# Optimization experiments

Measured on AMD Instinct MI355X. Metric: run time of the kernel, lower is better.

Reference implementation:

```python
import jax, jax.numpy as jnp
import numpy as np
from jax import lax

NMODES, STEP, DTAPS, NTAPS = 2, 5, 1001, 101
HID = 100
L_FIBER = 2000000.0
DZ = L_FIBER / STEP
GAMMA = 0.0016567
D_PARAM = 16.5
FC = 299792458.0 / 1.55e-6
FS_NOM = 160e9
B, SEQ = 4, 500000


def _get_beta2(D, Fc):
    c_kms = 299792458.0 / 1e3  # speed of light [km/s]
    lamb = c_kms / Fc          # wavelength [km]
    return -(D * lamb ** 2) / (2.0 * np.pi * c_kms)


def _dispersion_kernel(Fs):
    # Fs: [B] sampling rate in Hz -> time-domain dispersion kernel [B, DTAPS] complex64
    beta2 = _get_beta2(D_PARAM, FC) / 1000.0  # [s^2/m]
    beta1 = 0.0  # Fi == Fc so the walk-off term vanishes
    dz = -DZ     # module calls dispersion_kernel(-self.dz, ...)
    f = np.fft.fftfreq(DTAPS).astype(np.float32)
    omega = 2.0 * np.pi * Fs[:, None] * f  # [B, DTAPS] rad/s
    phase = (beta2 / 2.0) * omega ** 2 * dz + beta1 * omega * dz
    kf = jnp.exp(-1j * phase)  # freq-domain response, complex64
    return jnp.fft.fftshift(jnp.fft.ifft(kf, axis=-1), axes=-1).astype(jnp.complex64)


def _nonlinear_kernel(task_info, W1, b1, W2, b2):
    # hypernetwork-generated nonlinear kernel [B, NMODES, NMODES, NTAPS]
    scale = 1.0 / 200.0
    b = task_info.shape[0]
    Fs = task_info[:, 2] / FS_NOM
    Ts = (1.0 / Fs)[:, None, None]  # [B,1,1] (broadcasts over taps like expand)
    pos = jnp.abs(jnp.arange(-(NTAPS // 2), NTAPS // 2 + 1)).astype(jnp.float32)
    pos = pos[None, :, None] * scale  # [1,NTAPS,1]
    inp = pos * Ts ** 2               # [B,NTAPS,1]
    h = jax.nn.relu(inp @ W1 + b1)    # [B,NTAPS,HID]
    mlp_out = h @ W2 + b2             # [B,NTAPS,NMODES^2]
    k1 = Ts ** 2 * mlp_out * jnp.exp(-pos * Ts ** 2)
    return jnp.transpose(k1, (0, 2, 1)).reshape(b, NMODES, NMODES, NTAPS)


def _corr(x, h):
    # x:[B,M,L] real, h:[B,taps] -> valid cross-correlation [B,M,L-taps+1] (torch conv1d semantics)
    def one(xb, hb):
        return lax.conv_general_dilated(xb[:, None, :], hb[None, None, :], (1,), 'VALID')[:, 0]
    return jax.vmap(one)(x, h)


def _nconv(p, K):
    # p:[B,Min,L], K:[B,Mout,Min,taps] -> [B,Mout,L-taps+1]
    def one(pb, Kb):
        return lax.conv_general_dilated(pb[None], Kb, (1,), 'VALID')[0]
    return jax.vmap(one)(p, K)


def _forward(x_real, x_imag, task_info, W1, b1, W2, b2):
    P = 0.001 * 10.0 ** (task_info[:, 0] / 10.0) / NMODES  # launch power per mode [W]
    Dk = _dispersion_kernel(task_info[:, 2])
    hr, hi = jnp.real(Dk), jnp.imag(Dk)
    Nk = _nonlinear_kernel(task_info, W1, b1, W2, b2)
    xr = jnp.transpose(x_real, (0, 2, 1))  # [B,M,L]
    xi = jnp.transpose(x_imag, (0, 2, 1))
    trim = (NTAPS - 1) // 2
    coef = (GAMMA * DZ) * P[:, None, None]
    for _ in range(STEP):
        # complex dispersion conv: (xr+i xi) * (hr+i hi)
        ar = _corr(xr, hr) - _corr(xi, hi)
        ai = _corr(xr, hi) + _corr(xi, hr)
        # nonlinear phase from |x|^2 filtered by hypernet kernel
        phi = _nconv(ar ** 2 + ai ** 2, Nk)  # [B,M,L-ntaps+1]
        theta = phi * coef
        c, s = jnp.cos(theta), jnp.sin(theta)
        art = ar[:, :, trim:ar.shape[2] - trim]
        ait = ai[:, :, trim:ai.shape[2] - trim]
        # x * exp(i*theta)
        xr = art * c - ait * s
        xi = art * s + ait * c
    out = jnp.stack([xr, xi], axis=-1)      # [B,M,Lout,2]
    return jnp.transpose(out, (0, 2, 1, 3))  # [B,Lout,M,2] (real/imag stacked)


def setup_inputs() -> dict:
    key = jax.random.key(0)
    k = jax.random.split(key, 6)
    x_real = jax.random.normal(k[0], (B, SEQ, NMODES), jnp.float32)
    x_imag = jax.random.normal(k[1], (B, SEQ, NMODES), jnp.float32)
    Pdbm = jax.random.uniform(k[2], (B,), jnp.float32, -2.0, 2.0)
    task_info = jnp.stack([Pdbm,
                           jnp.full((B,), FC, jnp.float32),
                           jnp.full((B,), FS_NOM, jnp.float32),
                           jnp.ones((B,), jnp.float32)], axis=1)
    W1 = jax.random.normal(k[3], (1, HID), jnp.float32) * 0.5
    b1 = jnp.zeros((HID,), jnp.float32)
    W2 = jax.random.normal(k[4], (HID, NMODES * NMODES), jnp.float32) * 0.02
    b2 = jnp.zeros((NMODES * NMODES,), jnp.float32)
    return {"x_real": x_real, "x_imag": x_imag, "task_info": task_info,
            "W1": W1, "b1": b1, "W2": W2, "b2": b2}


def reference(x_real, x_imag, task_info, W1, b1, W2, b2):
    return _forward(x_real, x_imag, task_info, W1, b1, W2, b2)
```

## Files before the change

### kernel.cpp

```cpp
#include <hip/hip_runtime.h>

#define NM      2
#define STEPS_C 5
#define DTAPS_C 1001
#define NTAPS_C 101
#define HID_C   100
#define B_C     4
#define SEQ_C   500000
#define SSTR    SEQ_C
#define NKP     104
#define FS_NOM_D 160000000000.0
#define PI_D 3.14159265358979323846

#define SWZ(L) ((L) + ((((unsigned)(L)) >> 5) << 2))

#define LD4V(A0,A1,A2,A3, SRC) { float4 q_ = *(const float4*)&(SRC); \
    A0=q_.x; A1=q_.y; A2=q_.z; A3=q_.w; }

__device__ __forceinline__ void cmulf(float& o_r, float& o_i,
                                      float a_r, float a_i, float b_r, float b_i)
{ o_r = a_r * b_r - a_i * b_i; o_i = a_r * b_i + a_i * b_r; }

__global__ void build_disp(const float* __restrict__ task,
                           float* __restrict__ HR, float* __restrict__ HI)
{
    __shared__ double skr[DTAPS_C], ski[DTAPS_C];
    const int b = blockIdx.y;
    const double Fs = (double)task[b * 4 + 2];
    const double c_kms = 299792458.0 / 1000.0;
    const double Fc    = 299792458.0 / 1.55e-6;
    const double lamb  = c_kms / Fc;
    const double beta2 = -(16.5 * lamb * lamb) / (2.0 * PI_D * c_kms) / 1000.0;
    const double dz    = -400000.0;

    for (int k = threadIdx.x; k < DTAPS_C; k += blockDim.x) {
        double fk = ((k <= DTAPS_C / 2) ? (double)k : (double)(k - DTAPS_C)) / (double)DTAPS_C;
        double om = 2.0 * PI_D * Fs * fk;
        double ph = 0.5 * beta2 * om * om * dz;
        ph = fmod(ph, 2.0 * PI_D);
        double s, c; sincos(ph, &s, &c);
        skr[k] = c;  ski[k] = -s;
    }
    __syncthreads();

    const int ln = threadIdx.x >> 3;
    const int kp = threadIdx.x & 7;
    const int n  = blockIdx.x * 32 + ln;
    double dr = 0.0, di = 0.0;
    {
        const int nn = (n < DTAPS_C) ? n : 0;
        const int r0 = (nn * kp) % DTAPS_C;
        const int rs = (nn * 8) % DTAPS_C;
        double a0 = 2.0 * PI_D * (double)r0 / (double)DTAPS_C;
        double as = 2.0 * PI_D * (double)rs / (double)DTAPS_C;
        double s0, c0, ss, cs;
        sincos(a0, &s0, &c0);
        sincos(as, &ss, &cs);
        for (int k = kp; k < DTAPS_C; k += 8) {
            dr += skr[k] * c0 - ski[k] * s0;
            di += skr[k] * s0 + ski[k] * c0;
            const double nc = c0 * cs - s0 * ss;
            s0 = c0 * ss + s0 * cs;
            c0 = nc;
        }
    }
    #pragma unroll
    for (int m = 1; m <= 4; m <<= 1) {
        dr += __shfl_xor(dr, m, 64);
        di += __shfl_xor(di, m, 64);
    }
    if (kp == 0 && n < DTAPS_C) {
        int m = n + DTAPS_C / 2; if (m >= DTAPS_C) m -= DTAPS_C;
        HR[b * DTAPS_C + m] = (float)(dr / (double)DTAPS_C);
        HI[b * DTAPS_C + m] = (float)(di / (double)DTAPS_C);
    }
}

__global__ void build_G(const float* __restrict__ HR, const float* __restrict__ HI,
                        float* __restrict__ Gb)
{
    __shared__ float shr[DTAPS_C], shi[DTAPS_C];
    const int b = blockIdx.y;
    for (int k = threadIdx.x; k < DTAPS_C; k += blockDim.x) {
        shr[k] = HR[b * DTAPS_C + k];
        shi[k] = HI[b * DTAPS_C + k];
    }
    __syncthreads();

    const int ln = threadIdx.x >> 3;
    const int kp = threadIdx.x & 7;
    const int f  = blockIdx.x * 32 + ln;
    double ar = 0.0, ai = 0.0;
    {
        const int r0 = (f * kp) & 4095;
        const int rs = (f * 8) & 4095;
        double a0 = (2.0 * PI_D / 4096.0) * (double)r0;
        double as = (2.0 * PI_D / 4096.0) * (double)rs;
        double s0, c0, ss, cs;
        sincos(a0, &s0, &c0);
        sincos(as, &ss, &cs);
        for (int k = kp; k < DTAPS_C; k += 8) {
            const double hre = (double)shr[k], him = (double)shi[k];
            ar += hre * c0 - him * s0;
            ai += hre * s0 + him * c0;
            const double nc = c0 * cs - s0 * ss;
            s0 = c0 * ss + s0 * cs;
            c0 = nc;
        }
    }
    #pragma unroll
    for (int m = 1; m <= 4; m <<= 1) {
        ar += __shfl_xor(ar, m, 64);
        ai += __shfl_xor(ai, m, 64);
    }
    if (kp == 0) {
        const int p = ((f & 15) << 8) + (((f >> 4) & 15) << 4) + (f >> 8);
        Gb[(size_t)(b * 4096 + p) * 2 + 0] = (float)(ar * (1.0 / 4096.0));
        Gb[(size_t)(b * 4096 + p) * 2 + 1] = (float)(ai * (1.0 / 4096.0));
    }
}

__global__ void build_nk(const float* __restrict__ task,
                         const float* __restrict__ W1, const float* __restrict__ b1,
                         const float* __restrict__ W2, const float* __restrict__ b2,
                         float* __restrict__ NKg, float* __restrict__ COEF)
{
    const int tid = threadIdx.x;
    for (int i = tid; i < B_C * 4 * NKP; i += blockDim.x) NKg[i] = 0.f;
    if (tid < B_C) {
        float pdbm = task[tid * 4 + 0];
        float P = 0.001f * powf(10.f, pdbm * 0.1f) / (float)NM;
        COEF[tid] = (float)(0.0016567 * 400000.0) * P;
    }
    __syncthreads();
    if (tid < B_C * NTAPS_C) {
        const int b = tid / NTAPS_C, tap = tid % NTAPS_C;
        float Fsn = task[b * 4 + 2] * (float)(1.0 / FS_NOM_D);
        float Ts = 1.f / Fsn, Ts2 = Ts * Ts;
        float pos = fabsf((float)(tap - NTAPS_C / 2)) * (1.f / 200.f);
        float inp = pos * Ts2;
        float o0 = b2[0], o1 = b2[1], o2 = b2[2], o3 = b2[3];
        for (int j = 0; j < HID_C; ++j) {
            float h = fmaxf(fmaf(inp, W1[j], b1[j]), 0.f);
            o0 = fmaf(h, W2[j * 4 + 0], o0);
            o1 = fmaf(h, W2[j * 4 + 1], o1);
            o2 = fmaf(h, W2[j * 4 + 2], o2);
            o3 = fmaf(h, W2[j * 4 + 3], o3);
        }
        float sc = Ts2 * expf(-pos * Ts2);
        NKg[(b * 4 + 0) * NKP + tap] = o0 * sc;
        NKg[(b * 4 + 1) * NKP + tap] = o1 * sc;
        NKg[(b * 4 + 2) * NKP + tap] = o2 * sc;
        NKg[(b * 4 + 3) * NKP + tap] = o3 * sc;
    }
}

__global__ void transpose_in(const float* __restrict__ xr_in, const float* __restrict__ xi_in,
                             float* __restrict__ XR, float* __restrict__ XI)
{
    int idx = blockIdx.x * blockDim.x + threadIdx.x;
    if (idx >= B_C * SEQ_C) return;
    int b = idx / SEQ_C, t = idx - b * SEQ_C;
    float2 vr = ((const float2*)xr_in)[idx];
    float2 vi = ((const float2*)xi_in)[idx];
    XR[(size_t)(b * 2 + 0) * SSTR + t] = vr.x;
    XR[(size_t)(b * 2 + 1) * SSTR + t] = vr.y;
    XI[(size_t)(b * 2 + 0) * SSTR + t] = vi.x;
    XI[(size_t)(b * 2 + 1) * SSTR + t] = vi.y;
}

template<int SGN>
__device__ __forceinline__ void dft4(float& ar, float& ai, float& br, float& bi,
                                     float& cr, float& ci, float& dr, float& di)
{
    float t0r = ar + cr, t0i = ai + ci;
    float t1r = ar - cr, t1i = ai - ci;
    float t2r = br + dr, t2i = bi + di;
    float t3r = br - dr, t3i = bi - di;
    ar = t0r + t2r; ai = t0i + t2i;
    cr = t0r - t2r; ci = t0i - t2i;
    if (SGN < 0) {
        br = t1r + t3i; bi = t1i - t3r;
        dr = t1r - t3i; di = t1i + t3r;
    } else {
        br = t1r - t3i; bi = t1i + t3r;
        dr = t1r + t3i; di = t1i - t3r;
    }
}

template<int SGN>
__device__ __forceinline__ void tw16(float& r, float& i, float c, float s)
{
    float nr, ni;
    if (SGN < 0) { nr = r * c + i * s; ni = i * c - r * s; }
    else         { nr = r * c - i * s; ni = i * c + r * s; }
    r = nr; i = ni;
}

template<int SGN>
__device__ __forceinline__ void dft16(float (&xr)[16], float (&xi)[16])
{
    #pragma unroll
    for (int n1 = 0; n1 < 4; ++n1)
        dft4<SGN>(xr[n1], xi[n1], xr[n1+4], xi[n1+4],
                  xr[n1+8], xi[n1+8], xr[n1+12], xi[n1+12]);
    const float C1 = 0.923879532511286756f, S1 = 0.382683432365089772f;
    const float C2 = 0.707106781186547524f;
    tw16<SGN>(xr[5],  xi[5],  C1,  S1);
    tw16<SGN>(xr[9],  xi[9],  C2,  C2);
    tw16<SGN>(xr[13], xi[13], S1,  C1);
    tw16<SGN>(xr[6],  xi[6],  C2,  C2);
    tw16<SGN>(xr[10], xi[10], 0.f, 1.f);
    tw16<SGN>(xr[14], xi[14], -C2, C2);
    tw16<SGN>(xr[7],  xi[7],  S1,  C1);
    tw16<SGN>(xr[11], xi[11], -C2, C2);
    tw16<SGN>(xr[15], xi[15], -C1, -S1);
    #pragma unroll
    for (int k4 = 0; k4 < 4; ++k4)
        dft4<SGN>(xr[4*k4+0], xi[4*k4+0], xr[4*k4+1], xi[4*k4+1],
                  xr[4*k4+2], xi[4*k4+2], xr[4*k4+3], xi[4*k4+3]);
}

#define TWLADDER_INIT(c_, s_)                                              \
    float w1r_ = (c_), w1i_ = (s_), w2r_, w2i_, w3r_, w3i_, w4r_, w4i_;    \
    cmulf(w2r_, w2i_, w1r_, w1i_, w1r_, w1i_);                             \
    cmulf(w3r_, w3i_, w2r_, w2i_, w1r_, w1i_);                             \
    cmulf(w4r_, w4i_, w2r_, w2i_, w2r_, w2i_);                             \
    float bgr_ = 1.f, bgi_ = 0.f;

#define TWLADDER_GET(k_, twr_, twi_)                                       \
    {                                                                      \
        const int j_ = (k_) & 3;                                           \
        if      (j_ == 0) { twr_ = bgr_; twi_ = bgi_; }                    \
        else if (j_ == 1) cmulf(twr_, twi_, bgr_, bgi_, w1r_, w1i_);       \
        else if (j_ == 2) cmulf(twr_, twi_, bgr_, bgi_, w2r_, w2i_);       \
        else              cmulf(twr_, twi_, bgr_, bgi_, w3r_, w3i_);       \
    }

#define TWLADDER_STEP(k_)                                                  \
    if (((k_) & 3) == 3 && (k_) < 15) {                                    \
        float nr_, ni_;                                                    \
        cmulf(nr_, ni_, bgr_, bgi_, w4r_, w4i_);                           \
        bgr_ = nr_; bgi_ = ni_;                                            \
    }

#define FFTN  4096
#define FSTEP 3096
#define PH(i) ((i) + ((((unsigned)(i)) >> 5) << 1))
#define LDSN  4352

__global__ __launch_bounds__(256, 2) void disp_fft(
    const float* __restrict__ XR, const float* __restrict__ XI,
    const float* __restrict__ Gb,
    float* __restrict__ AR, float* __restrict__ AI, int La)
{
    __shared__ __align__(16) float sre[LDSN];
    __shared__ __align__(16) float sim[LDSN];
    const int t = threadIdx.x;
    const int seq = blockIdx.y;
    const int b = seq >> 1;
    const int tile0 = blockIdx.x * FSTEP;
    const int Lin = La + (DTAPS_C - 1);
    const int rem_in = Lin - tile0;
    const float* xr = XR + (size_t)seq * SSTR + tile0;
    const float* xi = XI + (size_t)seq * SSTR + tile0;

    #pragma unroll
    for (int q = 0; q < 4; ++q) {
        const int i0 = q * 1024 + t * 4;
        float4 vr4 = make_float4(0.f, 0.f, 0.f, 0.f);
        float4 vi4 = make_float4(0.f, 0.f, 0.f, 0.f);
        if (i0 + 3 < rem_in) {
            vr4 = *(const float4*)(xr + i0);
            vi4 = *(const float4*)(xi + i0);
        } else {
            if (i0 + 0 < rem_in) { vr4.x = xr[i0+0]; vi4.x = xi[i0+0]; }
            if (i0 + 1 < rem_in) { vr4.y = xr[i0+1]; vi4.y = xi[i0+1]; }
            if (i0 + 2 < rem_in) { vr4.z = xr[i0+2]; vi4.z = xi[i0+2]; }
        }
        const int p = PH(i0);
        sre[p+0] = vr4.x; sre[p+1] = vr4.y; sre[p+2] = vr4.z; sre[p+3] = vr4.w;
        sim[p+0] = vi4.x; sim[p+1] = vi4.y; sim[p+2] = vi4.z; sim[p+3] = vi4.w;
    }
    __syncthreads();

    float vr[16], vi[16];

    {
        const int base = PH(t);
        #pragma unroll
        for (int m = 0; m < 16; ++m) { vr[m] = sre[base + 272*m]; vi[m] = sim[base + 272*m]; }
        dft16<-1>(vr, vi);
        float s, c; sincosf((float)(-2.0 * PI_D / 4096.0) * (float)t, &s, &c);
        TWLADDER_INIT(c, s)
        #pragma unroll
        for (int k = 0; k < 16; ++k) {
            const int sl = 4*(k&3) + (k>>2);
            float twr, twi;
            TWLADDER_GET(k, twr, twi)
            sre[base + 272*k] = vr[sl]*twr - vi[sl]*twi;
            sim[base + 272*k] = vr[sl]*twi + vi[sl]*twr;
            TWLADDER_STEP(k)
        }
    }
    __syncthreads();

    {
        const int j = t & 15, blk = t >> 4;
        const int base = 272*blk + j;
        #pragma unroll
        for (int m = 0; m < 16; ++m) {
            const int o = base + 16*m + 2*(m>>1);
            vr[m] = sre[o]; vi[m] = sim[o];
        }
        dft16<-1>(vr, vi);
        float s, c; sincosf((float)(-2.0 * PI_D / 256.0) * (float)j, &s, &c);
        TWLADDER_INIT(c, s)
        #pragma unroll
        for (int k = 0; k < 16; ++k) {
            const int sl = 4*(k&3) + (k>>2);
            const int o = base + 16*k + 2*(k>>1);
            float twr, twi;
            TWLADDER_GET(k, twr, twi)
            sre[o] = vr[sl]*twr - vi[sl]*twi;
            sim[o] = vr[sl]*twi + vi[sl]*twr;
            TWLADDER_STEP(k)
        }
    }
    __syncthreads();

    {
        const int base = 16*t + 2*(t>>1);
        #pragma unroll
        for (int m = 0; m < 16; ++m) { vr[m] = sre[base + m]; vi[m] = sim[base + m]; }
        dft16<-1>(vr, vi);
        const float2* gp = ((const float2*)Gb) + ((size_t)b << 12) + (t << 4);
        float wr2[16], wi2[16];
        #pragma unroll
        for (int k = 0; k < 16; ++k) {
            const int sl = 4*(k&3) + (k>>2);
            const float2 g = gp[k];
            wr2[k] = vr[sl]*g.x - vi[sl]*g.y;
            wi2[k] = vr[sl]*g.y + vi[sl]*g.x;
        }
        dft16<1>(wr2, wi2);
        #pragma unroll
        for (int m = 0; m < 16; ++m) {
            const int sl = 4*(m&3) + (m>>2);
            sre[base + m] = wr2[sl]; sim[base + m] = wi2[sl];
        }
    }
    __syncthreads();

    {
        const int j = t & 15, blk = t >> 4;
        const int base = 272*blk + j;
        float s, c; sincosf((float)(2.0 * PI_D / 256.0) * (float)j, &s, &c);
        TWLADDER_INIT(c, s)
        #pragma unroll
        for (int k = 0; k < 16; ++k) {
            const int o = base + 16*k + 2*(k>>1);
            const float a = sre[o], d = sim[o];
            float twr, twi;
            TWLADDER_GET(k, twr, twi)
            vr[k] = a*twr - d*twi; vi[k] = a*twi + d*twr;
            TWLADDER_STEP(k)
        }
        dft16<1>(vr, vi);
        #pragma unroll
        for (int m = 0; m < 16; ++m) {
            const int sl = 4*(m&3) + (m>>2);
            const int o = base + 16*m + 2*(m>>1);
            sre[o] = vr[sl]; sim[o] = vi[sl];
        }
    }
    __syncthreads();

    {
        const int base = PH(t);
        float s, c; sincosf((float)(2.0 * PI_D / 4096.0) * (float)t, &s, &c);
        TWLADDER_INIT(c, s)
        #pragma unroll
        for (int k = 0; k < 16; ++k) {
            const float a = sre[base + 272*k], d = sim[base + 272*k];
            float twr, twi;
            TWLADDER_GET(k, twr, twi)
            vr[k] = a*twr - d*twi; vi[k] = a*twi + d*twr;
            TWLADDER_STEP(k)
        }
        dft16<1>(vr, vi);
        #pragma unroll
        for (int m = 0; m < 16; ++m) {
            const int sl = 4*(m&3) + (m>>2);
            sre[base + 272*m] = vr[sl]; sim[base + 272*m] = vi[sl];
        }
    }
    __syncthreads();

    const int nout = min(FSTEP, La - tile0);
    float* arp = AR + (size_t)seq * SSTR + tile0;
    float* aip = AI + (size_t)seq * SSTR + tile0;
    #pragma unroll
    for (int q = 0; q < 4; ++q) {
        const int i0 = q * 1024 + t * 4;
        if (i0 >= nout) continue;
        const int p = PH(i0);
        if (i0 + 3 < nout) {
            *(float4*)(arp + i0) = make_float4(sre[p], sre[p+1], sre[p+2], sre[p+3]);
            *(float4*)(aip + i0) = make_float4(sim[p], sim[p+1], sim[p+2], sim[p+3]);
        } else {
            for (int k = 0; k < 4; ++k) if (i0 + k < nout) {
                arp[i0+k] = sre[p+k]; aip[i0+k] = sim[p+k];
            }
        }
    }
}

#define K2_BLOCK 256
#define K2_TILE  2048
#define K2_LDSL  2176
#define K2_LDSP  2448

#define N_CH8(W_, V_, N_, P0, P1, KK)                                      \
  {                                                                        \
    LD4V(N_[0],N_[1],N_[2],N_[3], sp[P0]);                                 \
    LD4V(N_[4],N_[5],N_[6],N_[7], sp[P1]);                                 \
    _Pragma("unroll")                                                      \
    for (int d = 0; d < 8; ++d) {                                          \
      const float av = nkA[(KK) + d], bv = nkB[(KK) + d];                  \
      _Pragma("unroll")                                                    \
      for (int j = 0; j < 8; ++j) {                                        \
        const float xv = (j + d < 8) ? W_[j + d] : V_[j + d - 8];          \
        th0[j] = fmaf(av, xv, th0[j]);                                     \
        th1[j] = fmaf(bv, xv, th1[j]);                                     \
      }                                                                    \
    }                                                                      \
  }

__global__ __launch_bounds__(K2_BLOCK, 4) void nl_rotate(
    const float* __restrict__ AR, const float* __restrict__ AI,
    const float* __restrict__ NKg, const float* __restrict__ COEF,
    float* __restrict__ XR, float* __restrict__ XI,
    float* __restrict__ OUT, int Lb, int finalstep)
{
    __shared__ __align__(16) float sp0[K2_LDSP];
    __shared__ __align__(16) float sp1[K2_LDSP];
    const int b = blockIdx.y;
    const int tile0 = blockIdx.x * K2_TILE;
    const int nout  = min(K2_TILE, Lb - tile0);
    const int cnt   = nout + NTAPS_C - 1;
    const float* ar0 = AR + (size_t)(2 * b + 0) * SSTR + tile0;
    const float* ai0 = AI + (size_t)(2 * b + 0) * SSTR + tile0;
    const float* ar1 = AR + (size_t)(2 * b + 1) * SSTR + tile0;
    const float* ai1 = AI + (size_t)(2 * b + 1) * SSTR + tile0;

    for (int i0 = threadIdx.x * 4; i0 < K2_LDSL; i0 += K2_BLOCK * 4) {
        float4 p0v = make_float4(0.f, 0.f, 0.f, 0.f);
        float4 p1v = make_float4(0.f, 0.f, 0.f, 0.f);
        if (i0 + 3 < cnt) {
            float4 a4 = *(const float4*)(ar0 + i0);
            float4 c4 = *(const float4*)(ai0 + i0);
            float4 d4 = *(const float4*)(ar1 + i0);
            float4 e4 = *(const float4*)(ai1 + i0);
            p0v.x = fmaf(a4.x, a4.x, c4.x * c4.x);
            p0v.y = fmaf(a4.y, a4.y, c4.y * c4.y);
            p0v.z = fmaf(a4.z, a4.z, c4.z * c4.z);
            p0v.w = fmaf(a4.w, a4.w, c4.w * c4.w);
            p1v.x = fmaf(d4.x, d4.x, e4.x * e4.x);
            p1v.y = fmaf(d4.y, d4.y, e4.y * e4.y);
            p1v.z = fmaf(d4.z, d4.z, e4.z * e4.z);
            p1v.w = fmaf(d4.w, d4.w, e4.w * e4.w);
        } else {
            float p0a[4] = {0.f, 0.f, 0.f, 0.f};
            float p1a[4] = {0.f, 0.f, 0.f, 0.f};
            #pragma unroll
            for (int u = 0; u < 4; ++u) {
                const int i = i0 + u;
                if (i < cnt) {
                    float a = ar0[i], c = ai0[i];
                    float d = ar1[i], e = ai1[i];
                    p0a[u] = fmaf(a, a, c * c);
                    p1a[u] = fmaf(d, d, e * e);
                }
            }
            p0v = make_float4(p0a[0], p0a[1], p0a[2], p0a[3]);
            p1v = make_float4(p1a[0], p1a[1], p1a[2], p1a[3]);
        }
        const int p = SWZ(i0);
        *(float4*)&sp0[p] = p0v;
        *(float4*)&sp1[p] = p1v;
    }

    const int t0 = threadIdx.x * 8;
    float ra0[8], rb0[8], ra1[8], rb1[8];
    {
        const float* art0 = ar0 + t0 + NTAPS_C / 2;
        const float* ait0 = ai0 + t0 + NTAPS_C / 2;
        const float* art1 = ar1 + t0 + NTAPS_C / 2;
        const float* ait1 = ai1 + t0 + NTAPS_C / 2;
        #pragma unroll
        for (int j = 0; j < 8; ++j) {
            ra0[j] = art0[j]; rb0[j] = ait0[j];
            ra1[j] = art1[j]; rb1[j] = ait1[j];
        }
    }
    __syncthreads();

    if (t0 >= nout) return;

    float th0[8], th1[8];
    #pragma unroll
    for (int j = 0; j < 8; ++j) { th0[j] = 0.f; th1[j] = 0.f; }
    const float* nkb = NKg + b * 4 * NKP;

    const int a0 = SWZ(t0 + 16), a1 = SWZ(t0 + 20), a2 = SWZ(t0 + 24), a3 = SWZ(t0 + 28);
    const int a4 = SWZ(t0 + 32), a5 = SWZ(t0 + 36), a6 = SWZ(t0 + 40), a7 = SWZ(t0 + 44);

    for (int im = 0; im < 2; ++im) {
        const float* sp  = im ? sp1 : sp0;
        const float* nkA = nkb + (0 * 2 + im) * NKP;
        const float* nkB = nkb + (1 * 2 + im) * NKP;
        float U[8], V[8], N[8];
        LD4V(U[0],U[1],U[2],U[3], sp[SWZ(t0)]);
        LD4V(U[4],U[5],U[6],U[7], sp[SWZ(t0 + 4)]);
        LD4V(V[0],V[1],V[2],V[3], sp[SWZ(t0 + 8)]);
        LD4V(V[4],V[5],V[6],V[7], sp[SWZ(t0 + 12)]);
        N_CH8(U, V, N, a0,       a1,        0);
        N_CH8(V, N, U, a2,       a3,        8);
        N_CH8(N, U, V, a4,       a5,       16);
        N_CH8(U, V, N, a6,       a7,       24);
        N_CH8(V, N, U, a0 + 36,  a1 + 36,  32);
        N_CH8(N, U, V, a2 + 36,  a3 + 36,  40);
        N_CH8(U, V, N, a4 + 36,  a5 + 36,  48);
        N_CH8(V, N, U, a6 + 36,  a7 + 36,  56);
        N_CH8(N, U, V, a0 + 72,  a1 + 72,  64);
        N_CH8(U, V, N, a2 + 72,  a3 + 72,  72);
        N_CH8(V, N, U, a4 + 72,  a5 + 72,  80);
        N_CH8(N, U, V, a6 + 72,  a7 + 72,  88);
        N_CH8(U, V, N, a0 + 108, a1 + 108, 96);
    }

    const float coef = COEF[b];
    const int tg = tile0 + t0;

    float or0[8], oi0[8], or1[8], oi1[8];
    #pragma unroll
    for (int j = 0; j < 8; ++j) {
        float s0, c0, s1, c1;
        sincosf(th0[j] * coef, &s0, &c0);
        sincosf(th1[j] * coef, &s1, &c1);
        float a0v = ra0[j], b0v = rb0[j];
        float a1v = ra1[j], b1v = rb1[j];
        or0[j] = fmaf(a0v, c0, -b0v * s0);
        oi0[j] = fmaf(a0v, s0,  b0v * c0);
        or1[j] = fmaf(a1v, c1, -b1v * s1);
        oi1[j] = fmaf(a1v, s1,  b1v * c1);
    }

    const int rem = nout - t0;
    if (finalstep) {
        float4* op = (float4*)(OUT + (size_t)(b * Lb + tg) * 4);
        if (rem >= 8) {
            #pragma unroll
            for (int j = 0; j < 8; ++j) op[j] = make_float4(or0[j], oi0[j], or1[j], oi1[j]);
        } else {
            for (int j = 0; j < rem; ++j) op[j] = make_float4(or0[j], oi0[j], or1[j], oi1[j]);
        }
    } else {
        float* xr0 = XR + (size_t)(2 * b + 0) * SSTR + tg;
        float* xi0 = XI + (size_t)(2 * b + 0) * SSTR + tg;
        float* xr1 = XR + (size_t)(2 * b + 1) * SSTR + tg;
        float* xi1 = XI + (size_t)(2 * b + 1) * SSTR + tg;
        if (rem >= 8) {
            ((float4*)xr0)[0] = make_float4(or0[0], or0[1], or0[2], or0[3]);
            ((float4*)xr0)[1] = make_float4(or0[4], or0[5], or0[6], or0[7]);
            ((float4*)xi0)[0] = make_float4(oi0[0], oi0[1], oi0[2], oi0[3]);
            ((float4*)xi0)[1] = make_float4(oi0[4], oi0[5], oi0[6], oi0[7]);
            ((float4*)xr1)[0] = make_float4(or1[0], or1[1], or1[2], or1[3]);
            ((float4*)xr1)[1] = make_float4(or1[4], or1[5], or1[6], or1[7]);
            ((float4*)xi1)[0] = make_float4(oi1[0], oi1[1], oi1[2], oi1[3]);
            ((float4*)xi1)[1] = make_float4(oi1[4], oi1[5], oi1[6], oi1[7]);
        } else {
            for (int j = 0; j < rem; ++j) {
                xr0[j] = or0[j]; xi0[j] = oi0[j];
                xr1[j] = or1[j]; xi1[j] = oi1[j];
            }
        }
    }
}

extern "C" void kernel_launch(void* const* d_in, const int* in_sizes, int n_in,
                              void* d_out, int out_size, void* d_ws, size_t ws_size,
                              hipStream_t stream)
{
    const float* x_real = (const float*)d_in[0];
    const float* x_imag = (const float*)d_in[1];
    const float* task   = (const float*)d_in[2];
    const float* W1     = (const float*)d_in[3];
    const float* b1     = (const float*)d_in[4];
    const float* W2     = (const float*)d_in[5];
    const float* b2     = (const float*)d_in[6];
    float* out = (float*)d_out;
    float* ws  = (float*)d_ws;

    float* HR   = ws;
    float* HI   = HR + B_C * DTAPS_C;
    float* NKg  = HI + B_C * DTAPS_C;
    float* COEF = NKg + B_C * 4 * NKP;
    float* Gb   = ws + 16384;
    float* XR = ws + 16384 + 32768;
    float* XI = XR + (size_t)B_C * 2 * SEQ_C;
    float* AR = XI + (size_t)B_C * 2 * SEQ_C;
    float* AI = AR + (size_t)B_C * 2 * SEQ_C;

    build_disp<<<dim3(32, B_C), 256, 0, stream>>>(task, HR, HI);
    build_nk<<<1, 512, 0, stream>>>(task, W1, b1, W2, b2, NKg, COEF);
    build_G<<<dim3(128, B_C), 256, 0, stream>>>(HR, HI, Gb);
    {
        int n = B_C * SEQ_C;
        transpose_in<<<(n + 255) / 256, 256, 0, stream>>>(x_real, x_imag, XR, XI);
    }

    int L = SEQ_C;
    for (int s = 0; s < STEPS_C; ++s) {
        const int La = L - (DTAPS_C - 1);
        const int Lb = La - (NTAPS_C - 1);
        dim3 g1((La + FSTEP - 1) / FSTEP, B_C * NM);
        disp_fft<<<g1, 256, 0, stream>>>(XR, XI, Gb, AR, AI, La);
        dim3 g2((Lb + K2_TILE - 1) / K2_TILE, B_C);
        nl_rotate<<<g2, K2_BLOCK, 0, stream>>>(AR, AI, NKg, COEF, XR, XI, out,
                                               Lb, (s == STEPS_C - 1) ? 1 : 0);
        L = Lb;
    }
}
```

Before: 328.2 us.

## Give each wavefront its own LDS window to drop block-wide barrier in nl_rotate

The shared power-staging buffer in nl_rotate is split into per-wavefront windows of 512 outputs plus halo. Each wave loads and squares its own slice with overlapping halos, then waits on its own LDS writes instead of calling __syncthreads. This removes block-level synchronisation so waves can start the convolution independently. In exchange the halo regions are loaded redundantly (632 versus 512 elements per wave), and total LDS use rises slightly.

```diff
diff --git a/kernel.cpp b/kernel.cpp
--- a/kernel.cpp
+++ b/kernel.cpp
@@ -418,8 +418,9 @@
 
 #define K2_BLOCK 256
 #define K2_TILE  2048
-#define K2_LDSL  2176
-#define K2_LDSP  2448
+#define WOUT     512
+#define K2_WLDSL 632
+#define K2_WLDSP 720
 
 #define N_CH8(W_, V_, N_, P0, P1, KK)                                      \
   {                                                                        \
@@ -443,55 +444,66 @@
     float* __restrict__ XR, float* __restrict__ XI,
     float* __restrict__ OUT, int Lb, int finalstep)
 {
-    __shared__ __align__(16) float sp0[K2_LDSP];
-    __shared__ __align__(16) float sp1[K2_LDSP];
+    __shared__ __align__(16) float sw[4][2][K2_WLDSP];
     const int b = blockIdx.y;
     const int tile0 = blockIdx.x * K2_TILE;
     const int nout  = min(K2_TILE, Lb - tile0);
     const int cnt   = nout + NTAPS_C - 1;
+    const int w    = threadIdx.x >> 6;
+    const int lane = threadIdx.x & 63;
+    const int wbase = w * WOUT;
     const float* ar0 = AR + (size_t)(2 * b + 0) * SSTR + tile0;
     const float* ai0 = AI + (size_t)(2 * b + 0) * SSTR + tile0;
     const float* ar1 = AR + (size_t)(2 * b + 1) * SSTR + tile0;
     const float* ai1 = AI + (size_t)(2 * b + 1) * SSTR + tile0;
 
-    for (int i0 = threadIdx.x * 4; i0 < K2_LDSL; i0 += K2_BLOCK * 4) {
-        float4 p0v = make_float4(0.f, 0.f, 0.f, 0.f);
-        float4 p1v = make_float4(0.f, 0.f, 0.f, 0.f);
-        if (i0 + 3 < cnt) {
-            float4 a4 = *(const float4*)(ar0 + i0);
-            float4 c4 = *(const float4*)(ai0 + i0);
-            float4 d4 = *(const float4*)(ar1 + i0);
-            float4 e4 = *(const float4*)(ai1 + i0);
-            p0v.x = fmaf(a4.x, a4.x, c4.x * c4.x);
-            p0v.y = fmaf(a4.y, a4.y, c4.y * c4.y);
-            p0v.z = fmaf(a4.z, a4.z, c4.z * c4.z);
-            p0v.w = fmaf(a4.w, a4.w, c4.w * c4.w);
-            p1v.x = fmaf(d4.x, d4.x, e4.x * e4.x);
-            p1v.y = fmaf(d4.y, d4.y, e4.y * e4.y);
-            p1v.z = fmaf(d4.z, d4.z, e4.z * e4.z);
-            p1v.w = fmaf(d4.w, d4.w, e4.w * e4.w);
-        } else {
-            float p0a[4] = {0.f, 0.f, 0.f, 0.f};
-            float p1a[4] = {0.f, 0.f, 0.f, 0.f};
-            #pragma unroll
-            for (int u = 0; u < 4; ++u) {
-                const int i = i0 + u;
-                if (i < cnt) {
-                    float a = ar0[i], c = ai0[i];
-                    float d = ar1[i], e = ai1[i];
-                    p0a[u] = fmaf(a, a, c * c);
-                    p1a[u] = fmaf(d, d, e * e);
+    float* sp0 = sw[w][0];
+    float* sp1 = sw[w][1];
+
+    #pragma unroll
+    for (int q = 0; q < 3; ++q) {
+        const int i0 = q * 256 + lane * 4;
+        if (i0 < K2_WLDSL) {
+            const int gi = wbase + i0;
+            float4 p0v = make_float4(0.f, 0.f, 0.f, 0.f);
+            float4 p1v = make_float4(0.f, 0.f, 0.f, 0.f);
+            if (gi + 3 < cnt) {
+                float4 a4 = *(const float4*)(ar0 + gi);
+                float4 c4 = *(const float4*)(ai0 + gi);
+                float4 d4 = *(const float4*)(ar1 + gi);
+                float4 e4 = *(const float4*)(ai1 + gi);
+                p0v.x = fmaf(a4.x, a4.x, c4.x * c4.x);
+                p0v.y = fmaf(a4.y, a4.y, c4.y * c4.y);
+                p0v.z = fmaf(a4.z, a4.z, c4.z * c4.z);
+                p0v.w = fmaf(a4.w, a4.w, c4.w * c4.w);
+                p1v.x = fmaf(d4.x, d4.x, e4.x * e4.x);
+                p1v.y = fmaf(d4.y, d4.y, e4.y * e4.y);
+                p1v.z = fmaf(d4.z, d4.z, e4.z * e4.z);
+                p1v.w = fmaf(d4.w, d4.w, e4.w * e4.w);
+            } else {
+                float p0a[4] = {0.f, 0.f, 0.f, 0.f};
+                float p1a[4] = {0.f, 0.f, 0.f, 0.f};
+                #pragma unroll
+                for (int u = 0; u < 4; ++u) {
+                    const int i = gi + u;
+                    if (i < cnt) {
+                        float a = ar0[i], c = ai0[i];
+                        float d = ar1[i], e = ai1[i];
+                        p0a[u] = fmaf(a, a, c * c);
+                        p1a[u] = fmaf(d, d, e * e);
+                    }
                 }
+                p0v = make_float4(p0a[0], p0a[1], p0a[2], p0a[3]);
+                p1v = make_float4(p1a[0], p1a[1], p1a[2], p1a[3]);
             }
-            p0v = make_float4(p0a[0], p0a[1], p0a[2], p0a[3]);
-            p1v = make_float4(p1a[0], p1a[1], p1a[2], p1a[3]);
-        }
-        const int p = SWZ(i0);
-        *(float4*)&sp0[p] = p0v;
-        *(float4*)&sp1[p] = p1v;
-    }
-
-    const int t0 = threadIdx.x * 8;
+            const int p = SWZ(i0);
+            *(float4*)&sp0[p] = p0v;
+            *(float4*)&sp1[p] = p1v;
+        }
+    }
+
+    const int t0 = wbase + lane * 8;
+    const int lt0 = lane * 8;
     float ra0[8], rb0[8], ra1[8], rb1[8];
     {
         const float* art0 = ar0 + t0 + NTAPS_C / 2;
@@ -504,7 +516,9 @@
             ra1[j] = art1[j]; rb1[j] = ait1[j];
         }
     }
-    __syncthreads();
+
+    asm volatile("s_waitcnt lgkmcnt(0)" ::: "memory");
+    __builtin_amdgcn_sched_barrier(0);
 
     if (t0 >= nout) return;
 
@@ -513,18 +527,18 @@
     for (int j = 0; j < 8; ++j) { th0[j] = 0.f; th1[j] = 0.f; }
     const float* nkb = NKg + b * 4 * NKP;
 
-    const int a0 = SWZ(t0 + 16), a1 = SWZ(t0 + 20), a2 = SWZ(t0 + 24), a3 = SWZ(t0 + 28);
-    const int a4 = SWZ(t0 + 32), a5 = SWZ(t0 + 36), a6 = SWZ(t0 + 40), a7 = SWZ(t0 + 44);
+    const int a0 = SWZ(lt0 + 16), a1 = SWZ(lt0 + 20), a2 = SWZ(lt0 + 24), a3 = SWZ(lt0 + 28);
+    const int a4 = SWZ(lt0 + 32), a5 = SWZ(lt0 + 36), a6 = SWZ(lt0 + 40), a7 = SWZ(lt0 + 44);
 
     for (int im = 0; im < 2; ++im) {
         const float* sp  = im ? sp1 : sp0;
         const float* nkA = nkb + (0 * 2 + im) * NKP;
         const float* nkB = nkb + (1 * 2 + im) * NKP;
         float U[8], V[8], N[8];
-        LD4V(U[0],U[1],U[2],U[3], sp[SWZ(t0)]);
-        LD4V(U[4],U[5],U[6],U[7], sp[SWZ(t0 + 4)]);
-        LD4V(V[0],V[1],V[2],V[3], sp[SWZ(t0 + 8)]);
-        LD4V(V[4],V[5],V[6],V[7], sp[SWZ(t0 + 12)]);
+        LD4V(U[0],U[1],U[2],U[3], sp[SWZ(lt0)]);
+        LD4V(U[4],U[5],U[6],U[7], sp[SWZ(lt0 + 4)]);
+        LD4V(V[0],V[1],V[2],V[3], sp[SWZ(lt0 + 8)]);
+        LD4V(V[4],V[5],V[6],V[7], sp[SWZ(lt0 + 12)]);
         N_CH8(U, V, N, a0,       a1,        0);
         N_CH8(V, N, U, a2,       a3,        8);
         N_CH8(N, U, V, a4,       a5,       16);
```

New measurement: 323.9 us, median of 2. Within noise of the previous version (-1.3%).
